# Performance work log

Hardware: AMD Instinct MI355X
Metric: run time of the kernel (lower is better)

Reference implementation:

```python
import jax, jax.numpy as jnp
import numpy as np

N_NODES = 8192
IN_FEATS, H_FEATS, NUM_CLASSES = 512, 256, 16


def _glorot(key, shape):
    fan_in, fan_out = shape[0], shape[1]
    limit = float(np.sqrt(6.0 / (fan_in + fan_out)))
    return jax.random.uniform(key, shape, jnp.float32, -limit, limit)


def setup_inputs() -> dict:
    key = jax.random.key(0)
    ks = jax.random.split(key, 16)
    return {
        "x": jax.random.normal(ks[0], (N_NODES, IN_FEATS), jnp.float32),
        "w1": _glorot(ks[1], (IN_FEATS, H_FEATS)), "b1": jnp.zeros((H_FEATS,), jnp.float32),
        "w2": _glorot(ks[2], (H_FEATS, H_FEATS)), "b2": jnp.zeros((H_FEATS,), jnp.float32),
        "w3": _glorot(ks[3], (H_FEATS, 32)),      "b3": jnp.zeros((32,), jnp.float32),
        "t": _glorot(ks[4], (1, 1)), "theta": _glorot(ks[5], (1, 1)),
        "gw1": _glorot(ks[6], (32, 16)), "gb1": jnp.zeros((16,), jnp.float32),
        "gw2": _glorot(ks[7], (16, 8)),  "gb2": jnp.zeros((8,), jnp.float32),
        "lw1": _glorot(ks[8], (8, 16)),  "lb1": jnp.zeros((16,), jnp.float32),
        "lw2": _glorot(ks[9], (16, NUM_CLASSES)), "lb2": jnp.zeros((NUM_CLASSES,), jnp.float32),
    }


def _pairwise_dist(h):
    # Euclidean cdist(h, h): [N, N], stable sqrt with zero subgradient at d=0
    sq = jnp.sum(h * h, axis=1)
    d2 = jnp.maximum(sq[:, None] + sq[None, :] - 2.0 * (h @ h.T), 0.0)
    return jnp.where(d2 > 0.0, jnp.sqrt(jnp.where(d2 > 0.0, d2, 1.0)), 0.0)


def reference(x, w1, b1, w2, b2, w3, b3, t, theta, gw1, gb1, gw2, gb2, lw1, lb1, lw2, lb2):
    n = x.shape[0]
    # MLP encoder (dropout is eval-mode identity)
    h = jax.nn.relu(x @ w1 + b1)
    h = jax.nn.relu(h @ w2 + b2)
    h = h @ w3 + b3                                  # [N, 32]
    # latent dense graph: A = sigmoid(t * (cdist + theta)); all entries > 0 -> fully dense graph
    A = jax.nn.sigmoid(t[0, 0] * (_pairwise_dist(h) + theta[0, 0]))   # [N, N]
    inv_deg = 1.0 / n                                # norm='right', in-degree == N for dense graph
    # GraphConv: dst aggregates sum_src A[src,dst] * (h[src] @ W) then right-normalizes
    h = jax.nn.relu((A.T @ (h @ gw1)) * inv_deg + gb1)   # [N, 16]
    h = jax.nn.relu((A.T @ (h @ gw2)) * inv_deg + gb2)   # [N, 8]
    h = jax.nn.relu(h @ lw1 + lb1)
    return h @ lw2 + lb2                             # [N, num_classes]
```

## Files before the change

kernel.cpp:

```cpp
#include <hip/hip_runtime.h>

typedef __attribute__((ext_vector_type(8))) short short8;
typedef __attribute__((ext_vector_type(4))) float f32x4;
typedef __attribute__((ext_vector_type(4))) unsigned short u16x4;
typedef unsigned short u16;
typedef unsigned int u32;

#define MFMA16 __builtin_amdgcn_mfma_f32_16x16x32_bf16

__device__ __forceinline__ u16 f2bf(float f) {
    u32 u = __builtin_bit_cast(u32, f);
    return (u16)((u + 0x7FFFu + ((u >> 16) & 1u)) >> 16);
}

__device__ __forceinline__ void split2(float f, u16& hi, u16& lo) {
    u32 u = __builtin_bit_cast(u32, f);
    hi = (u16)(u >> 16);
    float hf = __builtin_bit_cast(float, u & 0xFFFF0000u);
    float r = f - hf;
    lo = (u16)(__builtin_bit_cast(u32, r) >> 16);
}

__device__ __forceinline__ int swzA(int row, int slot) {
    return row * 64 + ((slot ^ ((row >> 1) & 3)) << 4);
}

__global__ void __launch_bounds__(256) k_tr(const float* __restrict__ w, float* __restrict__ wt,
                                            int K, int N) {
    int idx = blockIdx.x * 256 + threadIdx.x;
    if (idx >= K * N) return;
    int k = idx / N, n = idx - k * N;
    wt[n * K + k] = w[idx];
}

template <int K, int BN, bool RELU>
__global__ void __launch_bounds__(256, 2) k_gemm(const float* __restrict__ A,
                                                 const float* __restrict__ Bt,
                                                 const float* __restrict__ bias,
                                                 float* __restrict__ C, const int N) {
    constexpr int NT = BN / 16;
    __shared__ __align__(16) char smem[16384];
    char* const Ah = smem;
    char* const Al = smem + 4096;
    char* const Bh = smem + 8192;
    char* const Bl = smem + 12288;
    const int tid = threadIdx.x, lane = tid & 63, w = tid >> 6;
    const int frow = lane & 15, fg = lane >> 4;
    const int m0 = blockIdx.x * 64, n0 = blockIdx.y * BN;
    const int srow = tid >> 2, sc = tid & 3;
    const int swa = swzA(srow, sc);
    const bool doB = (BN == 64) || (tid < 128);
    const float* gA = A + (m0 + srow) * K + sc * 8;
    const float* gB = Bt + (n0 + srow) * K + sc * 8;

    f32x4 acc[NT];
    float bv[NT];
#pragma unroll
    for (int nt = 0; nt < NT; nt++) {
        acc[nt] = {0.f, 0.f, 0.f, 0.f};
        bv[nt] = bias[n0 + nt * 16 + frow];
    }
    const int fra = swzA(w * 16 + frow, fg);
    int frb[NT];
#pragma unroll
    for (int nt = 0; nt < NT; nt++) frb[nt] = swzA(nt * 16 + frow, fg);

    for (int k0 = 0; k0 < K; k0 += 32) {
        f32x4 a0 = *(const f32x4*)(gA + k0);
        f32x4 a1 = *(const f32x4*)(gA + k0 + 4);
        f32x4 b0 = {0.f, 0.f, 0.f, 0.f}, b1 = {0.f, 0.f, 0.f, 0.f};
        if (doB) {
            b0 = *(const f32x4*)(gB + k0);
            b1 = *(const f32x4*)(gB + k0 + 4);
        }
        __syncthreads();
        {
            short8 ah8, al8;
#pragma unroll
            for (int i = 0; i < 4; i++) { u16 hh, ll; split2(a0[i], hh, ll); ah8[i] = (short)hh; al8[i] = (short)ll; }
#pragma unroll
            for (int i = 0; i < 4; i++) { u16 hh, ll; split2(a1[i], hh, ll); ah8[4 + i] = (short)hh; al8[4 + i] = (short)ll; }
            *(short8*)(Ah + swa) = ah8;
            *(short8*)(Al + swa) = al8;
        }
        if (doB) {
            short8 bh8, bl8;
#pragma unroll
            for (int i = 0; i < 4; i++) { u16 hh, ll; split2(b0[i], hh, ll); bh8[i] = (short)hh; bl8[i] = (short)ll; }
#pragma unroll
            for (int i = 0; i < 4; i++) { u16 hh, ll; split2(b1[i], hh, ll); bh8[4 + i] = (short)hh; bl8[4 + i] = (short)ll; }
            *(short8*)(Bh + swa) = bh8;
            *(short8*)(Bl + swa) = bl8;
        }
        __syncthreads();
        const short8 afh = *(const short8*)(Ah + fra);
        const short8 afl = *(const short8*)(Al + fra);
#pragma unroll
        for (int nt = 0; nt < NT; nt++) {
            const short8 bfh = *(const short8*)(Bh + frb[nt]);
            const short8 bfl = *(const short8*)(Bl + frb[nt]);
            acc[nt] = MFMA16(afh, bfh, acc[nt], 0, 0, 0);
            acc[nt] = MFMA16(afh, bfl, acc[nt], 0, 0, 0);
            acc[nt] = MFMA16(afl, bfh, acc[nt], 0, 0, 0);
        }
    }
#pragma unroll
    for (int nt = 0; nt < NT; nt++) {
#pragma unroll
        for (int r = 0; r < 4; r++) {
            float v = acc[nt][r] + bv[nt];
            if (RELU) v = fmaxf(v, 0.f);
            C[(m0 + w * 16 + fg * 4 + r) * N + (n0 + nt * 16 + frow)] = v;
        }
    }
}

__global__ void __launch_bounds__(256) k_post(const float* __restrict__ H,
                                              const float* __restrict__ gw1,
                                              u16* __restrict__ hhi, u16* __restrict__ hlo,
                                              float* __restrict__ sqv, u16* __restrict__ B1t) {
    __shared__ float gs[512];
    const int tid = threadIdx.x;
    gs[tid] = gw1[tid];
    gs[tid + 256] = gw1[tid + 256];
    __syncthreads();
    const int j = blockIdx.x * 256 + tid;
    float h[32];
#pragma unroll
    for (int q = 0; q < 8; q++) {
        f32x4 v = *(const f32x4*)(H + j * 32 + q * 4);
        h[q * 4 + 0] = v[0]; h[q * 4 + 1] = v[1]; h[q * 4 + 2] = v[2]; h[q * 4 + 3] = v[3];
    }
    float s = 0.f;
#pragma unroll
    for (int k = 0; k < 32; k++) s = fmaf(h[k], h[k], s);
    sqv[j] = s;
#pragma unroll
    for (int q = 0; q < 4; q++) {
        short8 vh, vl;
#pragma unroll
        for (int e = 0; e < 8; e++) {
            u16 hh, ll;
            split2(h[q * 8 + e], hh, ll);
            vh[e] = (short)hh; vl[e] = (short)ll;
        }
        *(short8*)(hhi + j * 32 + q * 8) = vh;
        *(short8*)(hlo + j * 32 + q * 8) = vl;
    }
    const float inv = 0.0001220703125f;
#pragma unroll
    for (int f = 0; f < 16; f++) {
        float a = 0.f;
#pragma unroll
        for (int k = 0; k < 32; k++) a = fmaf(h[k], gs[k * 16 + f], a);
        B1t[f * 8192 + j] = f2bf(a * inv);
    }
}

__global__ void __launch_bounds__(256, 2) k_agg(const u16* __restrict__ hhi,
                                                const u16* __restrict__ hlo,
                                                const float* __restrict__ sqv,
                                                const u16* __restrict__ Bt,
                                                float* __restrict__ P,
                                                const float* __restrict__ tp,
                                                const float* __restrict__ thp) {
    __shared__ __align__(16) char smem[25088];
    const int tid = threadIdx.x;
    const int lane = tid & 63;
    const int w = tid >> 6;
    const int frow = lane & 15, fg = lane >> 4;
    const int dstbase = blockIdx.x * 64;
    const int chunk = blockIdx.y;
    const float t = tp[0], th = thp[0];
    const float c1 = -t * 1.44269504088896340736f;
    const float c0 = c1 * th;

    char* const hdh_p = smem;
    char* const hdl_p = smem + 4096;
    char* const hsh_p = smem + 8192;
    char* const hsl_p = smem + 12288;
    float* const sqd = (float*)(smem + 16384);
    float* const sqs = (float*)(smem + 16640);
    char* const astr = smem + 16896 + w * 2048;

    const int srow = tid >> 2, sc = tid & 3;
    const int swa = swzA(srow, sc);

    {
        short8 vh = *(const short8*)(hhi + (dstbase + srow) * 32 + sc * 8);
        short8 vl = *(const short8*)(hlo + (dstbase + srow) * 32 + sc * 8);
        *(short8*)(hdh_p + swa) = vh;
        *(short8*)(hdl_p + swa) = vl;
        if (tid < 64) sqd[tid] = sqv[dstbase + tid];
    }
    __syncthreads();

    const int fra = swzA(w * 16 + frow, fg);
    const short8 hdh = *(const short8*)(hdh_p + fra);
    const short8 hdl = *(const short8*)(hdl_p + fra);
    const float sq_i = sqd[w * 16 + frow];
    const int il = w * 16 + frow;

    int hsfa[4], aw_off[4], ard[2];
#pragma unroll
    for (int jj = 0; jj < 4; jj++) hsfa[jj] = swzA(jj * 16 + frow, fg);
#pragma unroll
    for (int jj = 0; jj < 4; jj++)
        aw_off[jj] = frow * 128 + (((2 * jj + (fg >> 1)) ^ (frow & 7)) << 4) + ((fg & 1) << 3);
#pragma unroll
    for (int ks = 0; ks < 2; ks++) ard[ks] = frow * 128 + (((4 * ks + fg) ^ (frow & 7)) << 4);

    f32x4 outacc = {0.f, 0.f, 0.f, 0.f};
    const u16* bgp = Bt + frow * 8192;

    for (int jt = chunk * 16; jt < chunk * 16 + 16; ++jt) {
        const int jbase = jt * 64;
        const short8 bf0 = *(const short8*)(bgp + jbase + fg * 8);
        const short8 bf1 = *(const short8*)(bgp + jbase + 32 + fg * 8);
        const short8 vh = *(const short8*)(hhi + (jbase + srow) * 32 + sc * 8);
        const short8 vl = *(const short8*)(hlo + (jbase + srow) * 32 + sc * 8);
        const int il_cmp = (jbase == dstbase) ? il : -1;
        __syncthreads();
        *(short8*)(hsh_p + swa) = vh;
        *(short8*)(hsl_p + swa) = vl;
        if (tid < 64) sqs[tid] = sqv[jbase + tid];
        __syncthreads();

        short8 hsh[4], hsl[4];
#pragma unroll
        for (int jj = 0; jj < 4; jj++) {
            hsh[jj] = *(const short8*)(hsh_p + hsfa[jj]);
            hsl[jj] = *(const short8*)(hsl_p + hsfa[jj]);
        }
        f32x4 sacc[4];
#pragma unroll
        for (int jj = 0; jj < 4; jj++) {
            f32x4 z = {0.f, 0.f, 0.f, 0.f};
            z = MFMA16(hsh[jj], hdh, z, 0, 0, 0);
            z = MFMA16(hsh[jj], hdl, z, 0, 0, 0);
            z = MFMA16(hsl[jj], hdh, z, 0, 0, 0);
            sacc[jj] = z;
        }
#pragma unroll
        for (int jj = 0; jj < 4; jj++) {
            u16x4 av;
#pragma unroll
            for (int r = 0; r < 4; r++) {
                const int jl = jj * 16 + fg * 4 + r;
                const float sqj = sqs[jl];
                float d2 = fmaf(sacc[jj][r], -2.f, sq_i + sqj);
                d2 = fmaxf(d2, 0.f);
                float d = __builtin_amdgcn_sqrtf(d2);
                if (jl == il_cmp) d = 0.f;
                const float zz = fmaf(d, c1, c0);
                const float aa = __builtin_amdgcn_rcpf(1.f + __builtin_amdgcn_exp2f(zz));
                av[r] = f2bf(aa);
            }
            *(u16x4*)(astr + aw_off[jj]) = av;
        }
        const short8 af0 = *(const short8*)(astr + ard[0]);
        const short8 af1 = *(const short8*)(astr + ard[1]);
        outacc = MFMA16(af0, bf0, outacc, 0, 0, 0);
        outacc = MFMA16(af1, bf1, outacc, 0, 0, 0);
    }
#pragma unroll
    for (int r = 0; r < 4; r++) {
        const int ig = dstbase + w * 16 + fg * 4 + r;
        P[(chunk * 8192 + ig) * 16 + frow] = outacc[r];
    }
}

__global__ void __launch_bounds__(256) k_reduce1(const float* __restrict__ P,
                                                 const float* __restrict__ gw2,
                                                 const float* __restrict__ gb1,
                                                 u16* __restrict__ B2t) {
    __shared__ float gs[128];
    const int tid = threadIdx.x;
    if (tid < 128) gs[tid] = gw2[tid];
    __syncthreads();
    const int j = blockIdx.x * 256 + tid;
    float g[16];
#pragma unroll
    for (int q = 0; q < 4; q++) {
        f32x4 v = *(const f32x4*)(P + j * 16 + q * 4);
        g[q * 4 + 0] = v[0]; g[q * 4 + 1] = v[1]; g[q * 4 + 2] = v[2]; g[q * 4 + 3] = v[3];
    }
#pragma unroll
    for (int c = 1; c < 8; c++) {
#pragma unroll
        for (int q = 0; q < 4; q++) {
            f32x4 v = *(const f32x4*)(P + (c * 8192 + j) * 16 + q * 4);
            g[q * 4 + 0] += v[0]; g[q * 4 + 1] += v[1]; g[q * 4 + 2] += v[2]; g[q * 4 + 3] += v[3];
        }
    }
#pragma unroll
    for (int f = 0; f < 16; f++) g[f] = fmaxf(g[f] + gb1[f], 0.f);
    const float inv = 0.0001220703125f;
#pragma unroll
    for (int f2 = 0; f2 < 8; f2++) {
        float a = 0.f;
#pragma unroll
        for (int k = 0; k < 16; k++) a = fmaf(g[k], gs[k * 8 + f2], a);
        B2t[f2 * 8192 + j] = f2bf(a * inv);
    }
#pragma unroll
    for (int f2 = 8; f2 < 16; f2++) B2t[f2 * 8192 + j] = 0;
}

__global__ void __launch_bounds__(256) k_final(const float* __restrict__ P,
                                               const float* __restrict__ gb2,
                                               const float* __restrict__ lw1,
                                               const float* __restrict__ lb1,
                                               const float* __restrict__ lw2,
                                               const float* __restrict__ lb2,
                                               float* __restrict__ out) {
    __shared__ float s1[128], s2[256];
    const int tid = threadIdx.x;
    if (tid < 128) s1[tid] = lw1[tid];
    s2[tid] = lw2[tid];
    __syncthreads();
    const int j = blockIdx.x * 256 + tid;
    float g[8];
#pragma unroll
    for (int q = 0; q < 2; q++) {
        f32x4 v = *(const f32x4*)(P + j * 16 + q * 4);
        g[q * 4 + 0] = v[0]; g[q * 4 + 1] = v[1]; g[q * 4 + 2] = v[2]; g[q * 4 + 3] = v[3];
    }
#pragma unroll
    for (int c = 1; c < 8; c++) {
#pragma unroll
        for (int q = 0; q < 2; q++) {
            f32x4 v = *(const f32x4*)(P + (c * 8192 + j) * 16 + q * 4);
            g[q * 4 + 0] += v[0]; g[q * 4 + 1] += v[1]; g[q * 4 + 2] += v[2]; g[q * 4 + 3] += v[3];
        }
    }
#pragma unroll
    for (int f = 0; f < 8; f++) g[f] = fmaxf(g[f] + gb2[f], 0.f);
    float l1[16];
#pragma unroll
    for (int f = 0; f < 16; f++) {
        float a = lb1[f];
#pragma unroll
        for (int k = 0; k < 8; k++) a = fmaf(g[k], s1[k * 16 + f], a);
        l1[f] = fmaxf(a, 0.f);
    }
#pragma unroll
    for (int q = 0; q < 4; q++) {
        f32x4 v;
#pragma unroll
        for (int e = 0; e < 4; e++) {
            const int f = q * 4 + e;
            float a = lb2[f];
#pragma unroll
            for (int k = 0; k < 16; k++) a = fmaf(l1[k], s2[k * 16 + f], a);
            v[e] = a;
        }
        *(f32x4*)(out + j * 16 + q * 4) = v;
    }
}

extern "C" void kernel_launch(void* const* d_in, const int* in_sizes, int n_in,
                              void* d_out, int out_size, void* d_ws, size_t ws_size,
                              hipStream_t stream) {
    (void)in_sizes; (void)n_in; (void)out_size; (void)ws_size;
    const float* x   = (const float*)d_in[0];
    const float* w1  = (const float*)d_in[1];
    const float* b1  = (const float*)d_in[2];
    const float* w2  = (const float*)d_in[3];
    const float* b2  = (const float*)d_in[4];
    const float* w3  = (const float*)d_in[5];
    const float* b3  = (const float*)d_in[6];
    const float* t   = (const float*)d_in[7];
    const float* th  = (const float*)d_in[8];
    const float* gw1 = (const float*)d_in[9];
    const float* gb1 = (const float*)d_in[10];
    const float* gw2 = (const float*)d_in[11];
    const float* gb2 = (const float*)d_in[12];
    const float* lw1 = (const float*)d_in[13];
    const float* lb1 = (const float*)d_in[14];
    const float* lw2 = (const float*)d_in[15];
    const float* lb2 = (const float*)d_in[16];

    char* ws = (char*)d_ws;
    float* wt1 = (float*)(ws + 0);
    float* wt2 = (float*)(ws + 524288);
    float* wt3 = (float*)(ws + 786432);
    float* H1  = (float*)(ws + 819200);
    float* P   = (float*)(ws + 819200);
    float* H2  = (float*)(ws + 9207808);
    float* H   = (float*)(ws + 17596416);
    u16*   hhi = (u16*)(ws + 18644992);
    u16*   hlo = (u16*)(ws + 19169280);
    float* sqv = (float*)(ws + 19693568);
    u16*   B1t = (u16*)(ws + 19726336);
    u16*   B2t = (u16*)(ws + 19988480);

    k_tr<<<(512 * 256 + 255) / 256, 256, 0, stream>>>(w1, wt1, 512, 256);
    k_tr<<<(256 * 256 + 255) / 256, 256, 0, stream>>>(w2, wt2, 256, 256);
    k_tr<<<(256 * 32 + 255) / 256, 256, 0, stream>>>(w3, wt3, 256, 32);

    k_gemm<512, 64, true ><<<dim3(128, 4), 256, 0, stream>>>(x,  wt1, b1, H1, 256);
    k_gemm<256, 64, true ><<<dim3(128, 4), 256, 0, stream>>>(H1, wt2, b2, H2, 256);
    k_gemm<256, 32, false><<<dim3(128, 1), 256, 0, stream>>>(H2, wt3, b3, H, 32);

    k_post<<<32, 256, 0, stream>>>(H, gw1, hhi, hlo, sqv, B1t);

    k_agg<<<dim3(128, 8), 256, 0, stream>>>(hhi, hlo, sqv, B1t, P, t, th);
    k_reduce1<<<32, 256, 0, stream>>>(P, gw2, gb1, B2t);
    k_agg<<<dim3(128, 8), 256, 0, stream>>>(hhi, hlo, sqv, B2t, P, t, th);
    k_final<<<32, 256, 0, stream>>>(P, gb2, lw1, lb1, lw2, lb2, (float*)d_out);
}
```

Before: 140.1 us.

## Prefetch next source tile into registers and split aggregation into half-tile stages

Restructures the k_agg loop so the next 64-row source tile and its squared norms are loaded into registers while the current tile is computed. Shared memory shrinks because destination rows are now read directly from global memory instead of being staged. The per-tile work is split into two 32-column halves that interleave MFMA, the elementwise sigmoid and the A·B MFMA. The code also uses packed v_cvt_pk_bf16_f32 conversion, vector loads of the norms, and drops the 2-blocks-per-CU launch bound. Register pressure rises with the prefetch, and the extra occupancy hint is removed, which may change how many blocks fit per CU.

```diff
diff --git a/kernel.cpp b/kernel.cpp
--- a/kernel.cpp
+++ b/kernel.cpp
@@ -2,7 +2,7 @@
 
 typedef __attribute__((ext_vector_type(8))) short short8;
 typedef __attribute__((ext_vector_type(4))) float f32x4;
-typedef __attribute__((ext_vector_type(4))) unsigned short u16x4;
+typedef __attribute__((ext_vector_type(2))) unsigned int u32x2;
 typedef unsigned short u16;
 typedef unsigned int u32;
 
@@ -157,111 +157,103 @@
     }
 }
 
-__global__ void __launch_bounds__(256, 2) k_agg(const u16* __restrict__ hhi,
-                                                const u16* __restrict__ hlo,
-                                                const float* __restrict__ sqv,
-                                                const u16* __restrict__ Bt,
-                                                float* __restrict__ P,
-                                                const float* __restrict__ tp,
-                                                const float* __restrict__ thp) {
-    __shared__ __align__(16) char smem[25088];
-    const int tid = threadIdx.x;
-    const int lane = tid & 63;
-    const int w = tid >> 6;
+__device__ __forceinline__ void ew_pack(char* astr, int awoff, const f32x4 s, const f32x4 sq4,
+                                        float sq_i, float c0, float c1, int jloc, int il_cmp) {
+    float p[4];
+#pragma unroll
+    for (int r = 0; r < 4; r++) {
+        float d2 = fmaf(s[r], -2.f, sq_i + sq4[r]);
+        d2 = fmaxf(d2, 0.f);
+        float d = __builtin_amdgcn_sqrtf(d2);
+        if (jloc + r == il_cmp) d = 0.f;
+        const float z = fmaf(d, c1, c0);
+        p[r] = __builtin_amdgcn_rcpf(1.f + __builtin_amdgcn_exp2f(z));
+    }
+    u32 w0, w1;
+    asm("v_cvt_pk_bf16_f32 %0, %1, %2" : "=v"(w0) : "v"(p[0]), "v"(p[1]));
+    asm("v_cvt_pk_bf16_f32 %0, %1, %2" : "=v"(w1) : "v"(p[2]), "v"(p[3]));
+    u32x2 pk = {w0, w1};
+    *(u32x2*)(astr + awoff) = pk;
+}
+
+__global__ void __launch_bounds__(256) k_agg(const u16* __restrict__ hhi, const u16* __restrict__ hlo,
+                                             const float* __restrict__ sqv, const u16* __restrict__ Bt,
+                                             float* __restrict__ P,
+                                             const float* __restrict__ tp, const float* __restrict__ thp) {
+    __shared__ __align__(16) char smem[16640];
+    char* const bufh = smem;
+    char* const bufl = smem + 4096;
+    float* const sqb = (float*)(smem + 8192);
+    char* const astr0 = smem + 8448;
+
+    const int tid = threadIdx.x, lane = tid & 63, w = tid >> 6;
     const int frow = lane & 15, fg = lane >> 4;
     const int dstbase = blockIdx.x * 64;
     const int chunk = blockIdx.y;
     const float t = tp[0], th = thp[0];
     const float c1 = -t * 1.44269504088896340736f;
     const float c0 = c1 * th;
-
-    char* const hdh_p = smem;
-    char* const hdl_p = smem + 4096;
-    char* const hsh_p = smem + 8192;
-    char* const hsl_p = smem + 12288;
-    float* const sqd = (float*)(smem + 16384);
-    float* const sqs = (float*)(smem + 16640);
-    char* const astr = smem + 16896 + w * 2048;
+    char* const astr = astr0 + w * 2048;
 
     const int srow = tid >> 2, sc = tid & 3;
     const int swa = swzA(srow, sc);
 
-    {
-        short8 vh = *(const short8*)(hhi + (dstbase + srow) * 32 + sc * 8);
-        short8 vl = *(const short8*)(hlo + (dstbase + srow) * 32 + sc * 8);
-        *(short8*)(hdh_p + swa) = vh;
-        *(short8*)(hdl_p + swa) = vl;
-        if (tid < 64) sqd[tid] = sqv[dstbase + tid];
-    }
-    __syncthreads();
-
-    const int fra = swzA(w * 16 + frow, fg);
-    const short8 hdh = *(const short8*)(hdh_p + fra);
-    const short8 hdl = *(const short8*)(hdl_p + fra);
-    const float sq_i = sqd[w * 16 + frow];
+    const int igf = dstbase + w * 16 + frow;
+    const short8 hdh = *(const short8*)(hhi + igf * 32 + fg * 8);
+    const short8 hdl = *(const short8*)(hlo + igf * 32 + fg * 8);
+    const float sq_i = sqv[igf];
     const int il = w * 16 + frow;
 
-    int hsfa[4], aw_off[4], ard[2];
-#pragma unroll
-    for (int jj = 0; jj < 4; jj++) hsfa[jj] = swzA(jj * 16 + frow, fg);
+    int awo[4], ard[2];
 #pragma unroll
     for (int jj = 0; jj < 4; jj++)
-        aw_off[jj] = frow * 128 + (((2 * jj + (fg >> 1)) ^ (frow & 7)) << 4) + ((fg & 1) << 3);
-#pragma unroll
-    for (int ks = 0; ks < 2; ks++) ard[ks] = frow * 128 + (((4 * ks + fg) ^ (frow & 7)) << 4);
+        awo[jj] = frow * 128 + (((2 * jj + (fg >> 1)) ^ (frow & 7)) << 4) + ((fg & 1) << 3);
+#pragma unroll
+    for (int h = 0; h < 2; h++) ard[h] = frow * 128 + (((4 * h + fg) ^ (frow & 7)) << 4);
 
     f32x4 outacc = {0.f, 0.f, 0.f, 0.f};
-    const u16* bgp = Bt + frow * 8192;
-
-    for (int jt = chunk * 16; jt < chunk * 16 + 16; ++jt) {
-        const int jbase = jt * 64;
-        const short8 bf0 = *(const short8*)(bgp + jbase + fg * 8);
-        const short8 bf1 = *(const short8*)(bgp + jbase + 32 + fg * 8);
-        const short8 vh = *(const short8*)(hhi + (jbase + srow) * 32 + sc * 8);
-        const short8 vl = *(const short8*)(hlo + (jbase + srow) * 32 + sc * 8);
+
+    const int jb0 = chunk * 16 * 64;
+    short8 pvh = *(const short8*)(hhi + (jb0 + srow) * 32 + sc * 8);
+    short8 pvl = *(const short8*)(hlo + (jb0 + srow) * 32 + sc * 8);
+    float psq = 0.f;
+    if (tid < 64) psq = sqv[jb0 + tid];
+
+    for (int jtl = 0; jtl < 16; ++jtl) {
+        const int jbase = (chunk * 16 + jtl) * 64;
+        __syncthreads();
+        *(short8*)(bufh + swa) = pvh;
+        *(short8*)(bufl + swa) = pvl;
+        if (tid < 64) sqb[tid] = psq;
+        if (jtl + 1 < 16) {
+            const int jn = jbase + 64;
+            pvh = *(const short8*)(hhi + (jn + srow) * 32 + sc * 8);
+            pvl = *(const short8*)(hlo + (jn + srow) * 32 + sc * 8);
+            if (tid < 64) psq = sqv[jn + tid];
+        }
+        __syncthreads();
         const int il_cmp = (jbase == dstbase) ? il : -1;
-        __syncthreads();
-        *(short8*)(hsh_p + swa) = vh;
-        *(short8*)(hsl_p + swa) = vl;
-        if (tid < 64) sqs[tid] = sqv[jbase + tid];
-        __syncthreads();
-
-        short8 hsh[4], hsl[4];
-#pragma unroll
-        for (int jj = 0; jj < 4; jj++) {
-            hsh[jj] = *(const short8*)(hsh_p + hsfa[jj]);
-            hsl[jj] = *(const short8*)(hsl_p + hsfa[jj]);
-        }
-        f32x4 sacc[4];
-#pragma unroll
-        for (int jj = 0; jj < 4; jj++) {
-            f32x4 z = {0.f, 0.f, 0.f, 0.f};
-            z = MFMA16(hsh[jj], hdh, z, 0, 0, 0);
-            z = MFMA16(hsh[jj], hdl, z, 0, 0, 0);
-            z = MFMA16(hsl[jj], hdh, z, 0, 0, 0);
-            sacc[jj] = z;
-        }
-#pragma unroll
-        for (int jj = 0; jj < 4; jj++) {
-            u16x4 av;
-#pragma unroll
-            for (int r = 0; r < 4; r++) {
-                const int jl = jj * 16 + fg * 4 + r;
-                const float sqj = sqs[jl];
-                float d2 = fmaf(sacc[jj][r], -2.f, sq_i + sqj);
-                d2 = fmaxf(d2, 0.f);
-                float d = __builtin_amdgcn_sqrtf(d2);
-                if (jl == il_cmp) d = 0.f;
-                const float zz = fmaf(d, c1, c0);
-                const float aa = __builtin_amdgcn_rcpf(1.f + __builtin_amdgcn_exp2f(zz));
-                av[r] = f2bf(aa);
-            }
-            *(u16x4*)(astr + aw_off[jj]) = av;
-        }
-        const short8 af0 = *(const short8*)(astr + ard[0]);
-        const short8 af1 = *(const short8*)(astr + ard[1]);
-        outacc = MFMA16(af0, bf0, outacc, 0, 0, 0);
-        outacc = MFMA16(af1, bf1, outacc, 0, 0, 0);
+#pragma unroll
+        for (int h = 0; h < 2; ++h) {
+            const short8 hs0h = *(const short8*)(bufh + swzA(h * 32 + frow, fg));
+            const short8 hs0l = *(const short8*)(bufl + swzA(h * 32 + frow, fg));
+            const short8 hs1h = *(const short8*)(bufh + swzA(h * 32 + 16 + frow, fg));
+            const short8 hs1l = *(const short8*)(bufl + swzA(h * 32 + 16 + frow, fg));
+            const f32x4 sq0 = *(const f32x4*)(sqb + h * 32 + fg * 4);
+            const f32x4 sq1 = *(const f32x4*)(sqb + h * 32 + 16 + fg * 4);
+            const short8 bfh = *(const short8*)(Bt + frow * 8192 + jbase + h * 32 + fg * 8);
+            f32x4 s0 = {0.f, 0.f, 0.f, 0.f}, s1 = {0.f, 0.f, 0.f, 0.f};
+            s0 = MFMA16(hs0h, hdh, s0, 0, 0, 0);
+            s0 = MFMA16(hs0h, hdl, s0, 0, 0, 0);
+            s0 = MFMA16(hs0l, hdh, s0, 0, 0, 0);
+            s1 = MFMA16(hs1h, hdh, s1, 0, 0, 0);
+            s1 = MFMA16(hs1h, hdl, s1, 0, 0, 0);
+            s1 = MFMA16(hs1l, hdh, s1, 0, 0, 0);
+            ew_pack(astr, awo[2 * h], s0, sq0, sq_i, c0, c1, (2 * h) * 16 + fg * 4, il_cmp);
+            ew_pack(astr, awo[2 * h + 1], s1, sq1, sq_i, c0, c1, (2 * h + 1) * 16 + fg * 4, il_cmp);
+            const short8 af = *(const short8*)(astr + ard[h]);
+            outacc = MFMA16(af, bfh, outacc, 0, 0, 0);
+        }
     }
 #pragma unroll
     for (int r = 0; r < 4; r++) {
```

Measured after the change: 135.6 us. 3.2% less time.
